# Kernel optimization log

Measured on AMD Instinct MI355X. Metric: run time of the kernel, lower is better.

## Reference

```python
import jax, jax.numpy as jnp
import numpy as np

N, E, D, L = 50000, 800000, 128, 3

def setup_inputs() -> dict:
    key = jax.random.key(0)
    ks = jax.random.split(key, 6)
    X = jax.random.normal(ks[0], (N, D), dtype=jnp.float32)
    edge_index = jax.random.randint(ks[1], (2, E), 0, N, dtype=jnp.int64)
    eps = jax.random.normal(ks[2], (L,), dtype=jnp.float32)
    # Glorot-ish scaling for stability
    W1 = jax.random.normal(ks[3], (L, D, D), dtype=jnp.float32) / np.sqrt(D)
    b1 = jnp.zeros((L, D), dtype=jnp.float32)
    W2 = jax.random.normal(ks[4], (L, D, D), dtype=jnp.float32) / np.sqrt(D)
    b2 = jnp.zeros((L, D), dtype=jnp.float32)
    return {"X": X, "edge_index": edge_index, "eps": eps,
            "W1": W1, "b1": b1, "W2": W2, "b2": b2}

def reference(X, edge_index, eps, W1, b1, W2, b2):
    src = edge_index[0]  # message sources j (flow source_to_target)
    dst = edge_index[1]  # aggregation targets i
    n = X.shape[0]
    for i in range(L):  # fixed small layer loop
        X0 = X
        # propagate: gather X_j over edges, scatter-add to targets
        S = jax.ops.segment_sum(X[src], dst, num_segments=n)  # [N, D]
        Z = (1.0 + eps[i]) * X + S
        # MLP: Linear -> ReLU -> Linear
        H = jnp.maximum(Z @ W1[i] + b1[i], 0.0)
        X = H @ W2[i] + b2[i]
        X = X + X0  # residual=True
    return X
```

## Files before the change

### kernel.cpp

```cpp
#include <hip/hip_runtime.h>

#define NN 50000
#define NE 800000
#define DD 128
#define NL 3
#define ELLW 64
#define MT_TOTAL (NN / 16)
#define EDGE_BLKS ((NE + 255) / 256)
#define PACK_BLKS ((6 * 2048 + 255) / 256)
#define INIT_BLKS ((NN * DD / 8 + 255) / 256)

typedef short bf16x8 __attribute__((ext_vector_type(8)));
typedef float f32x4 __attribute__((ext_vector_type(4)));
typedef _Float16 half8 __attribute__((ext_vector_type(8)));
typedef unsigned short u16x8 __attribute__((ext_vector_type(8)));

__device__ __forceinline__ unsigned short f2bf(float x) {
  unsigned u = __float_as_uint(x);
  u += 0x7FFFu + ((u >> 16) & 1u);
  return (unsigned short)(u >> 16);
}
__device__ __forceinline__ float bf2f(unsigned short h) {
  return __uint_as_float(((unsigned)h) << 16);
}
__device__ __forceinline__ void cvt8(const float* zz, bf16x8* hi, bf16x8* lo) {
#pragma unroll
  for (int i = 0; i < 8; ++i) {
    unsigned short h = f2bf(zz[i]);
    (*hi)[i] = (short)h;
    (*lo)[i] = (short)f2bf(zz[i] - bf2f(h));
  }
}

__global__ __launch_bounds__(256) void prologue_k(
    const int* __restrict__ ei, int* __restrict__ cnt, unsigned short* __restrict__ ell,
    const float* __restrict__ W1, const float* __restrict__ W2,
    unsigned short* __restrict__ Wp,
    const float* __restrict__ X, _Float16* __restrict__ Xh)
{
  int b = blockIdx.x;
  if (b < EDGE_BLKS) {
    int e = b * 256 + threadIdx.x;
    if (e < NE) {
      int s = ei[e];
      int d = ei[NE + e];
      int pos = atomicAdd(&cnt[d], 1);
      if (pos < ELLW) ell[(size_t)d * ELLW + pos] = (unsigned short)s;
    }
  } else if (b < EDGE_BLKS + PACK_BLKS) {
    int t = (b - EDGE_BLKS) * 256 + threadIdx.x;
    if (t < 6 * 2048) {
      int m = t >> 11;
      int rem = t & 2047;
      int l = rem & 63;
      int ntks = rem >> 6;
      int ks = ntks & 3, nt = ntks >> 2;
      const float* W = (m < 3) ? (W1 + (size_t)m * DD * DD) : (W2 + (size_t)(m - 3) * DD * DD);
      int col = nt * 16 + (l & 15);
      int k0 = ks * 32 + (l >> 4) * 8;
      unsigned short* hi = Wp + (size_t)m * 2 * DD * DD + (size_t)rem * 8;
      unsigned short* lo = hi + DD * DD;
#pragma unroll
      for (int i = 0; i < 8; ++i) {
        float w = W[(size_t)(k0 + i) * DD + col];
        unsigned short h = f2bf(w);
        hi[i] = h;
        lo[i] = f2bf(w - bf2f(h));
      }
    }
  } else {
    int t = (b - EDGE_BLKS - PACK_BLKS) * 256 + threadIdx.x;
    if (t < NN * DD / 8) {
      const float4* p = (const float4*)X + (size_t)t * 2;
      float4 a = p[0], bb = p[1];
      half8 h;
      h[0] = (_Float16)a.x;  h[1] = (_Float16)a.y;  h[2] = (_Float16)a.z;  h[3] = (_Float16)a.w;
      h[4] = (_Float16)bb.x; h[5] = (_Float16)bb.y; h[6] = (_Float16)bb.z; h[7] = (_Float16)bb.w;
      *(half8*)(Xh + (size_t)t * 8) = h;
    }
  }
}

template<int OUT_F32>
__global__ __launch_bounds__(256) void fused_layer_k(
    const _Float16* __restrict__ Xh_in,
    const int* __restrict__ cnt, const unsigned short* __restrict__ ell,
    const float* __restrict__ eps, int layer,
    const unsigned short* __restrict__ Wp1, const float* __restrict__ b1,
    const unsigned short* __restrict__ Wp2, const float* __restrict__ b2,
    float* __restrict__ Xf_out, _Float16* __restrict__ Xh_out)
{
  __shared__ float ztile[16 * 132];
  __shared__ unsigned short rtile[16 * 136];
  const int w = threadIdx.x >> 6, l = threadIdx.x & 63;
  const int mt = blockIdx.x;
  const int c = l & 15, grp = l >> 4;

  {
    const float e1 = 1.0f + eps[layer];
    const int nl = w * 4 + grp;
    const int node = mt * 16 + nl;
    int deg = cnt[node]; deg = deg > ELLW ? ELLW : deg;
    const unsigned short* el = ell + (size_t)node * ELLW;
    const u16x8* el8 = (const u16x8*)el;
    float acc[8];
    {
      half8 sv = *(const half8*)(Xh_in + (size_t)node * DD + c * 8);
#pragma unroll
      for (int i = 0; i < 8; ++i) acc[i] = e1 * (float)sv[i];
      *(u16x8*)(rtile + nl * 136 + c * 8) = *(const u16x8*)&sv;
    }
    int nf8 = deg >> 3;
    u16x8 nxt;
    if (nf8) nxt = el8[0];
    for (int t = 0; t < nf8; ++t) {
      u16x8 cur = nxt;
      if (t + 1 < nf8) nxt = el8[t + 1];
      half8 v0 = *(const half8*)(Xh_in + (size_t)cur[0] * DD + c * 8);
      half8 v1 = *(const half8*)(Xh_in + (size_t)cur[1] * DD + c * 8);
      half8 v2 = *(const half8*)(Xh_in + (size_t)cur[2] * DD + c * 8);
      half8 v3 = *(const half8*)(Xh_in + (size_t)cur[3] * DD + c * 8);
      half8 v4 = *(const half8*)(Xh_in + (size_t)cur[4] * DD + c * 8);
      half8 v5 = *(const half8*)(Xh_in + (size_t)cur[5] * DD + c * 8);
      half8 v6 = *(const half8*)(Xh_in + (size_t)cur[6] * DD + c * 8);
      half8 v7 = *(const half8*)(Xh_in + (size_t)cur[7] * DD + c * 8);
#pragma unroll
      for (int i = 0; i < 8; ++i)
        acc[i] += (((float)v0[i] + (float)v1[i]) + ((float)v2[i] + (float)v3[i]))
                + (((float)v4[i] + (float)v5[i]) + ((float)v6[i] + (float)v7[i]));
    }
    for (int j = nf8 * 8; j < deg; ++j) {
      half8 v = *(const half8*)(Xh_in + (size_t)el[j] * DD + c * 8);
#pragma unroll
      for (int i = 0; i < 8; ++i) acc[i] += (float)v[i];
    }
    float* dst = ztile + nl * 132 + c * 8;
    *(float4*)dst = make_float4(acc[0], acc[1], acc[2], acc[3]);
    *(float4*)(dst + 4) = make_float4(acc[4], acc[5], acc[6], acc[7]);
  }
  __syncthreads();

  f32x4 acc1[2];
#pragma unroll
  for (int nt = 0; nt < 2; ++nt) acc1[nt] = (f32x4){0.f, 0.f, 0.f, 0.f};
  {
    const float* arow = ztile + (l & 15) * 132;
    const unsigned short* Whi = Wp1;
    const unsigned short* Wlo = Wp1 + DD * DD;
#pragma unroll
    for (int ks = 0; ks < 4; ++ks) {
      const float* zp = arow + ks * 32 + grp * 8;
      float zz[8] = {zp[0], zp[1], zp[2], zp[3], zp[4], zp[5], zp[6], zp[7]};
      bf16x8 ahi, alo; cvt8(zz, &ahi, &alo);
#pragma unroll
      for (int nt = 0; nt < 2; ++nt) {
        int ntb = w * 2 + nt;
        size_t off = ((size_t)(ntb * 4 + ks) * 64 + l) * 8;
        bf16x8 bhi = *(const bf16x8*)(Whi + off);
        bf16x8 blo = *(const bf16x8*)(Wlo + off);
        acc1[nt] = __builtin_amdgcn_mfma_f32_16x16x32_bf16(ahi, bhi, acc1[nt], 0, 0, 0);
        acc1[nt] = __builtin_amdgcn_mfma_f32_16x16x32_bf16(ahi, blo, acc1[nt], 0, 0, 0);
        acc1[nt] = __builtin_amdgcn_mfma_f32_16x16x32_bf16(alo, bhi, acc1[nt], 0, 0, 0);
      }
    }
  }
  __syncthreads();

  {
#pragma unroll
    for (int nt = 0; nt < 2; ++nt) {
      int ntb = w * 2 + nt;
      float bv = b1[ntb * 16 + c];
#pragma unroll
      for (int r = 0; r < 4; ++r)
        ztile[(grp * 4 + r) * 132 + ntb * 16 + c] = fmaxf(acc1[nt][r] + bv, 0.f);
    }
  }
  __syncthreads();

  f32x4 acc2[2];
#pragma unroll
  for (int nt = 0; nt < 2; ++nt) acc2[nt] = (f32x4){0.f, 0.f, 0.f, 0.f};
  {
    const float* arow = ztile + (l & 15) * 132;
    const unsigned short* Whi = Wp2;
    const unsigned short* Wlo = Wp2 + DD * DD;
#pragma unroll
    for (int ks = 0; ks < 4; ++ks) {
      const float* hp = arow + ks * 32 + grp * 8;
      float hh[8] = {hp[0], hp[1], hp[2], hp[3], hp[4], hp[5], hp[6], hp[7]};
      bf16x8 ahi, alo; cvt8(hh, &ahi, &alo);
#pragma unroll
      for (int nt = 0; nt < 2; ++nt) {
        int ntb = w * 2 + nt;
        size_t off = ((size_t)(ntb * 4 + ks) * 64 + l) * 8;
        bf16x8 bhi = *(const bf16x8*)(Whi + off);
        bf16x8 blo = *(const bf16x8*)(Wlo + off);
        acc2[nt] = __builtin_amdgcn_mfma_f32_16x16x32_bf16(ahi, bhi, acc2[nt], 0, 0, 0);
        acc2[nt] = __builtin_amdgcn_mfma_f32_16x16x32_bf16(ahi, blo, acc2[nt], 0, 0, 0);
        acc2[nt] = __builtin_amdgcn_mfma_f32_16x16x32_bf16(alo, bhi, acc2[nt], 0, 0, 0);
      }
    }
#pragma unroll
    for (int nt = 0; nt < 2; ++nt) {
      int ntb = w * 2 + nt;
      int col = ntb * 16 + c;
      float bv = b2[col];
#pragma unroll
      for (int r = 0; r < 4; ++r) {
        int row = grp * 4 + r;
        int node = mt * 16 + row;
        size_t idx = (size_t)node * DD + col;
        unsigned short rb = rtile[row * 136 + col];
        float rv = (float)(*(_Float16*)&rb);
        float v = acc2[nt][r] + bv + rv;
        if (OUT_F32) Xf_out[idx] = v;
        else         Xh_out[idx] = (_Float16)v;
      }
    }
  }
}

extern "C" void kernel_launch(void* const* d_in, const int* in_sizes, int n_in,
                              void* d_out, int out_size, void* d_ws, size_t ws_size,
                              hipStream_t stream) {
  const float* X   = (const float*)d_in[0];
  const int*   ei  = (const int*)d_in[1];
  const float* eps = (const float*)d_in[2];
  const float* W1  = (const float*)d_in[3];
  const float* b1  = (const float*)d_in[4];
  const float* W2  = (const float*)d_in[5];
  const float* b2  = (const float*)d_in[6];
  float* Xout = (float*)d_out;

  char* ws = (char*)d_ws;
  size_t off = 0;
  int* cnt = (int*)(ws + off); off += 256 * (((size_t)NN * 4 + 255) / 256);
  unsigned short* ell = (unsigned short*)(ws + off); off += (size_t)NN * ELLW * 2;
  unsigned short* Wp = (unsigned short*)(ws + off); off += (size_t)6 * 2 * DD * DD * 2;
  off = 256 * ((off + 255) / 256);
  _Float16* Xh0 = (_Float16*)(ws + off); off += (size_t)NN * DD * 2;
  _Float16* Xh1 = (_Float16*)(ws + off); off += (size_t)NN * DD * 2;

  hipMemsetAsync(cnt, 0, NN * 4, stream);
  prologue_k<<<EDGE_BLKS + PACK_BLKS + INIT_BLKS, 256, 0, stream>>>(
      ei, cnt, ell, W1, W2, Wp, X, Xh0);

  const int fgrid = MT_TOTAL;
  fused_layer_k<0><<<fgrid, 256, 0, stream>>>(Xh0, cnt, ell, eps, 0,
      Wp + (size_t)0 * 2 * DD * DD, b1 + 0 * DD,
      Wp + (size_t)3 * 2 * DD * DD, b2 + 0 * DD, nullptr, Xh1);
  fused_layer_k<0><<<fgrid, 256, 0, stream>>>(Xh1, cnt, ell, eps, 1,
      Wp + (size_t)1 * 2 * DD * DD, b1 + 1 * DD,
      Wp + (size_t)4 * 2 * DD * DD, b2 + 1 * DD, nullptr, Xh0);
  fused_layer_k<1><<<fgrid, 256, 0, stream>>>(Xh0, cnt, ell, eps, 2,
      Wp + (size_t)2 * 2 * DD * DD, b1 + 2 * DD,
      Wp + (size_t)5 * 2 * DD * DD, b2 + 2 * DD, Xout, nullptr);
}
```

Measured before the change: 193.4 us.

## Partition nodes by XCD so ELL build and layer blocks stay L2-local

Block indices are remapped so each of the 8 XCDs (blockIdx round-robin) owns a contiguous range of node tiles in the ELL build, the fp16 conversion and all fused layer kernels. The edge scatter now has every XCD scan all edges and keep only destinations in its own node range, so atomics and ELL writes hit the local L2. The cost is that each XCD reads the whole edge list, 8 reads in total instead of one, and some blocks return early as padding. Neighbour gathers across partitions still miss L2.

```diff
diff --git a/kernel.cpp b/kernel.cpp
--- a/kernel.cpp
+++ b/kernel.cpp
@@ -6,9 +6,12 @@
 #define NL 3
 #define ELLW 64
 #define MT_TOTAL (NN / 16)
-#define EDGE_BLKS ((NE + 255) / 256)
+#define MT_PER_XCD 391
+#define NODES_PER_XCD (MT_PER_XCD * 16)
+#define SCAT_BLKS (MT_PER_XCD * 8)
+#define SCAT_CHUNK 2048
 #define PACK_BLKS ((6 * 2048 + 255) / 256)
-#define INIT_BLKS ((NN * DD / 8 + 255) / 256)
+#define INIT_BLKS 3128
 
 typedef short bf16x8 __attribute__((ext_vector_type(8)));
 typedef float f32x4 __attribute__((ext_vector_type(4)));
@@ -39,16 +42,36 @@
     const float* __restrict__ X, _Float16* __restrict__ Xh)
 {
   int b = blockIdx.x;
-  if (b < EDGE_BLKS) {
-    int e = b * 256 + threadIdx.x;
-    if (e < NE) {
-      int s = ei[e];
-      int d = ei[NE + e];
-      int pos = atomicAdd(&cnt[d], 1);
-      if (pos < ELLW) ell[(size_t)d * ELLW + pos] = (unsigned short)s;
-    }
-  } else if (b < EDGE_BLKS + PACK_BLKS) {
-    int t = (b - EDGE_BLKS) * 256 + threadIdx.x;
+  if (b < SCAT_BLKS) {
+    int g = b & 7, chunk = b >> 3;
+    int lo = g * NODES_PER_XCD, hi = lo + NODES_PER_XCD;
+    int base = chunk * SCAT_CHUNK + threadIdx.x * 8;
+    if (base + 7 < NE) {
+      int4 d0 = *(const int4*)(ei + NE + base);
+      int4 d1 = *(const int4*)(ei + NE + base + 4);
+      int4 s0 = *(const int4*)(ei + base);
+      int4 s1 = *(const int4*)(ei + base + 4);
+      int dd[8] = {d0.x, d0.y, d0.z, d0.w, d1.x, d1.y, d1.z, d1.w};
+      int ss[8] = {s0.x, s0.y, s0.z, s0.w, s1.x, s1.y, s1.z, s1.w};
+#pragma unroll
+      for (int i = 0; i < 8; ++i) {
+        int d = dd[i];
+        if (d >= lo && d < hi) {
+          int pos = atomicAdd(&cnt[d], 1);
+          if (pos < ELLW) ell[(size_t)d * ELLW + pos] = (unsigned short)ss[i];
+        }
+      }
+    } else {
+      for (int e = base; e < NE; ++e) {
+        int d = ei[NE + e];
+        if (d >= lo && d < hi) {
+          int pos = atomicAdd(&cnt[d], 1);
+          if (pos < ELLW) ell[(size_t)d * ELLW + pos] = (unsigned short)ei[e];
+        }
+      }
+    }
+  } else if (b < SCAT_BLKS + PACK_BLKS) {
+    int t = (b - SCAT_BLKS) * 256 + threadIdx.x;
     if (t < 6 * 2048) {
       int m = t >> 11;
       int rem = t & 2047;
@@ -69,14 +92,17 @@
       }
     }
   } else {
-    int t = (b - EDGE_BLKS - PACK_BLKS) * 256 + threadIdx.x;
-    if (t < NN * DD / 8) {
-      const float4* p = (const float4*)X + (size_t)t * 2;
-      float4 a = p[0], bb = p[1];
+    int bb = b - SCAT_BLKS - PACK_BLKS;
+    int g = bb & 7, ii = bb >> 3;
+    int mt = g * MT_PER_XCD + ii;
+    if (mt < MT_TOTAL) {
+      size_t base = (size_t)mt * 16 * DD + threadIdx.x * 8;
+      const float4* p = (const float4*)(X + base);
+      float4 a = p[0], bb2 = p[1];
       half8 h;
-      h[0] = (_Float16)a.x;  h[1] = (_Float16)a.y;  h[2] = (_Float16)a.z;  h[3] = (_Float16)a.w;
-      h[4] = (_Float16)bb.x; h[5] = (_Float16)bb.y; h[6] = (_Float16)bb.z; h[7] = (_Float16)bb.w;
-      *(half8*)(Xh + (size_t)t * 8) = h;
+      h[0] = (_Float16)a.x;   h[1] = (_Float16)a.y;   h[2] = (_Float16)a.z;   h[3] = (_Float16)a.w;
+      h[4] = (_Float16)bb2.x; h[5] = (_Float16)bb2.y; h[6] = (_Float16)bb2.z; h[7] = (_Float16)bb2.w;
+      *(half8*)(Xh + base) = h;
     }
   }
 }
@@ -92,8 +118,9 @@
 {
   __shared__ float ztile[16 * 132];
   __shared__ unsigned short rtile[16 * 136];
+  const int mt = (blockIdx.x & 7) * MT_PER_XCD + (blockIdx.x >> 3);
+  if (mt >= MT_TOTAL) return;
   const int w = threadIdx.x >> 6, l = threadIdx.x & 63;
-  const int mt = blockIdx.x;
   const int c = l & 15, grp = l >> 4;
 
   {
@@ -243,10 +270,10 @@
   _Float16* Xh1 = (_Float16*)(ws + off); off += (size_t)NN * DD * 2;
 
   hipMemsetAsync(cnt, 0, NN * 4, stream);
-  prologue_k<<<EDGE_BLKS + PACK_BLKS + INIT_BLKS, 256, 0, stream>>>(
+  prologue_k<<<SCAT_BLKS + PACK_BLKS + INIT_BLKS, 256, 0, stream>>>(
       ei, cnt, ell, W1, W2, Wp, X, Xh0);
 
-  const int fgrid = MT_TOTAL;
+  const int fgrid = MT_PER_XCD * 8;
   fused_layer_k<0><<<fgrid, 256, 0, stream>>>(Xh0, cnt, ell, eps, 0,
       Wp + (size_t)0 * 2 * DD * DD, b1 + 0 * DD,
       Wp + (size_t)3 * 2 * DD * DD, b2 + 0 * DD, nullptr, Xh1);
```

Result: faster. 186.8 us (-3.4%).
